# Kernel optimization log

Measured on AMD Instinct MI355X. Metric: run time of the kernel, lower is better.

## Reference

```python
import jax, jax.numpy as jnp
import numpy as np

B, S, HID = 2, 2048, 4096
NH, NKV, D = 32, 8, 128
GROUPS = NH // NKV  # 4 query heads per KV head
THETA = 10000.0
MAX_SEQ = 4096


def _rope_tables():
    half = D // 2
    inv_freq = 1.0 / (THETA ** (np.arange(half, dtype=np.float32) / half))
    t = np.arange(MAX_SEQ, dtype=np.float32)
    freqs = np.outer(t, inv_freq)  # [MAX_SEQ, D//2]
    return jnp.asarray(np.cos(freqs)), jnp.asarray(np.sin(freqs))

ROPE_COS, ROPE_SIN = _rope_tables()


def _apply_rope(x, cos, sin):
    # x: [B, S, H, D]; cos/sin: [S, D//2]; half-split (NeoX) rotation as in _apply_rope_inline
    half = x.shape[-1] // 2
    x0, x1 = x[..., :half], x[..., half:]
    c = cos[None, :, None, :]
    s = sin[None, :, None, :]
    return jnp.concatenate([x0 * c - x1 * s, x0 * s + x1 * c], axis=-1)


def setup_inputs() -> dict:
    key = jax.random.key(0)
    ks = jax.random.split(key, 5)
    wscale = 1.0 / np.sqrt(HID).astype(np.float32)  # keep activations O(1)
    return {
        "x": jax.random.normal(ks[0], (B, S, HID), dtype=jnp.float32),
        "positions": jnp.arange(S, dtype=jnp.int32),
        "w_q": jax.random.normal(ks[1], (NH * D, HID), dtype=jnp.float32) * wscale,
        "w_k": jax.random.normal(ks[2], (NKV * D, HID), dtype=jnp.float32) * wscale,
        "w_v": jax.random.normal(ks[3], (NKV * D, HID), dtype=jnp.float32) * wscale,
        "w_o": jax.random.normal(ks[4], (HID, NH * D), dtype=jnp.float32) * wscale,
    }


def reference(x, positions, w_q, w_k, w_v, w_o):
    cos = ROPE_COS[positions]  # [S, D//2]
    sin = ROPE_SIN[positions]
    # Separate Q/K/V projections (no bias), as in the training forward()
    q = (x @ w_q.T).reshape(B, S, NH, D)
    k = (x @ w_k.T).reshape(B, S, NKV, D)
    v = (x @ w_v.T).reshape(B, S, NKV, D)
    q = _apply_rope(q, cos, sin)
    k = _apply_rope(k, cos, sin)
    # [B, H, S, D] layout
    q = q.transpose(0, 2, 1, 3)
    k = k.transpose(0, 2, 1, 3)
    v = v.transpose(0, 2, 1, 3)
    # GQA: group query heads over shared KV heads instead of repeating K/V
    qg = q.reshape(B, NKV, GROUPS, S, D)
    scale = 1.0 / jnp.sqrt(jnp.float32(D))
    scores = jnp.einsum("bkgqd,bkmd->bkgqm", qg, k) * scale  # [B, NKV, G, Sq, Skv]
    causal = jnp.tril(jnp.ones((S, S), dtype=bool))
    scores = jnp.where(causal[None, None, None], scores, jnp.float32(-jnp.inf))
    probs = jax.nn.softmax(scores, axis=-1)
    ctx = jnp.einsum("bkgqm,bkmd->bkgqd", probs, v)  # [B, NKV, G, S, D]
    ctx = ctx.reshape(B, NH, S, D).transpose(0, 2, 1, 3).reshape(B, S, NH * D)
    return ctx @ w_o.T
```

## Files before the change

### kernel.cpp

```cpp
#include <hip/hip_runtime.h>
#include <math.h>

typedef short s16x8 __attribute__((ext_vector_type(8)));
typedef float f32x4 __attribute__((ext_vector_type(4)));
typedef unsigned u32x4 __attribute__((ext_vector_type(4)));
typedef unsigned short u16;

#define S_LEN 2048
#define HID_DIM 4096
#define NH_Q 32
#define NKV_H 8
#define DHEAD 128

__device__ __forceinline__ u16 f2bf(float f) {
  unsigned u = __builtin_bit_cast(unsigned, f);
  u += 0x7fffu + ((u >> 16) & 1u);
  return (u16)(u >> 16);
}

__device__ __forceinline__ void gload16(const u16* g, u16* l) {
  __builtin_amdgcn_global_load_lds(
      (const __attribute__((address_space(1))) void*)g,
      (__attribute__((address_space(3))) void*)l, 16, 0, 0);
}

__global__ void cvt_kernel(const float* __restrict__ in, u16* __restrict__ out, int n4) {
  int stride = gridDim.x * blockDim.x;
  for (int i = blockIdx.x * blockDim.x + threadIdx.x; i < n4; i += stride) {
    float4 f = ((const float4*)in)[i];
    uint2 o;
    o.x = (unsigned)f2bf(f.x) | ((unsigned)f2bf(f.y) << 16);
    o.y = (unsigned)f2bf(f.z) | ((unsigned)f2bf(f.w) << 16);
    ((uint2*)out)[i] = o;
  }
}

__global__ void cvt_all_kernel(const float* __restrict__ x, const float* __restrict__ wq,
                               const float* __restrict__ wk, const float* __restrict__ wv,
                               const float* __restrict__ wo, u16* __restrict__ x_bf,
                               u16* __restrict__ wqkv_bf, u16* __restrict__ wo_bf,
                               const int* __restrict__ positions, float* __restrict__ cos_t,
                               float* __restrict__ sin_t, int with_wo) {
  const int R0 = 4194304, R1 = 8388608, R2 = 9437184, R3 = 10485760, R4 = 14680064;
  const int cvt_end = with_wo ? R4 : R3;
  const int rope_units = 32768;
  const int total = cvt_end + rope_units;
  const int stride = gridDim.x * blockDim.x;
  for (int i = blockIdx.x * blockDim.x + threadIdx.x; i < total; i += stride) {
    if (i < cvt_end) {
      const float* src;
      u16* dst;
      int off;
      if (i < R0)      { src = x;  dst = x_bf;               off = i; }
      else if (i < R1) { src = wq; dst = wqkv_bf;            off = i - R0; }
      else if (i < R2) { src = wk; dst = wqkv_bf + 16777216; off = i - R1; }
      else if (i < R3) { src = wv; dst = wqkv_bf + 20971520; off = i - R2; }
      else             { src = wo; dst = wo_bf;              off = i - R3; }
      float4 f = ((const float4*)src)[off];
      uint2 o;
      o.x = (unsigned)f2bf(f.x) | ((unsigned)f2bf(f.y) << 16);
      o.y = (unsigned)f2bf(f.z) | ((unsigned)f2bf(f.w) << 16);
      ((uint2*)dst)[off] = o;
    } else {
      int base = (i - cvt_end) * 4;
#pragma unroll
      for (int e = 0; e < 4; ++e) {
        int idx = base + e;
        int s = idx >> 6, j = idx & 63;
        float pos = (float)positions[s];
        float inv = expf(-(float)j * (9.210340371976184f / 64.0f));
        float sv, cv;
        sincosf(pos * inv, &sv, &cv);
        cos_t[idx] = cv;
        sin_t[idx] = sv;
      }
    }
  }
}

__global__ void rope_table_kernel(const int* __restrict__ positions,
                                  float* __restrict__ cos_t, float* __restrict__ sin_t) {
  int idx = blockIdx.x * 256 + threadIdx.x;
  if (idx >= S_LEN * 64) return;
  int s = idx >> 6, j = idx & 63;
  float pos = (float)positions[s];
  float inv = expf(-(float)j * (9.210340371976184f / 64.0f));
  float sv, cv;
  sincosf(pos * inv, &sv, &cv);
  cos_t[idx] = cv;
  sin_t[idx] = sv;
}

template<int EPI>
__global__ __launch_bounds__(512, 2) void gemmp_kernel(
    const u16* __restrict__ A, const u16* __restrict__ B,
    void* __restrict__ outp, int M, int N, int K,
    const float* __restrict__ cos_t, const float* __restrict__ sin_t) {
  __shared__ u16 LDS[73728];
  const int t = threadIdx.x;
  const int wave = t >> 6, lane = t & 63;
  const int l15 = lane & 15, lhi = lane >> 4;
  const int wr = wave >> 2, wc = wave & 3;
  const int gx = gridDim.x;
  const int nwg = gx * gridDim.y;
  const int id = blockIdx.y * gx + blockIdx.x;
  const int xcd = id & 7, cid = id >> 3;
  const int npx = gx >> 3;
  const int gy = nwg / gx;
  const int bxi = xcd * npx + cid / gy;
  const int byi = cid % gy;
  const int bm = byi * 128, bn = bxi * 256;

  const int sw = l15 & 7;
  int aoff[4][2], boff[2][2];
#pragma unroll
  for (int q = 0; q < 4; ++q)
#pragma unroll
    for (int ks = 0; ks < 2; ++ks)
      aoff[q][ks] = wr * 4096 + (q * 16 + l15) * 64 + (((ks << 2) + lhi) ^ sw) * 8;
#pragma unroll
  for (int f = 0; f < 2; ++f)
#pragma unroll
    for (int ks = 0; ks < 2; ++ks)
      boff[f][ks] = (f * 64 + wc * 16 + l15) * 64 + (((ks << 2) + lhi) ^ sw) * 8;

  const int lr1 = t >> 3;
  const int cs1 = ((t & 7) ^ (lr1 & 7)) * 8;
  const int ldsw = wave * 512;

  const f32x4 fz = {0.f, 0.f, 0.f, 0.f};
  f32x4 acc[4][4];
#pragma unroll
  for (int mf = 0; mf < 4; ++mf)
#pragma unroll
    for (int nf = 0; nf < 4; ++nf) acc[mf][nf] = fz;

  auto stageA = [&](int tile, int buf) {
    const size_t kb = (size_t)tile * 64;
    gload16(A + (size_t)(bm + lr1) * K + kb + cs1, &LDS[buf * 8192 + ldsw]);
    gload16(A + (size_t)(bm + 64 + lr1) * K + kb + cs1, &LDS[buf * 8192 + 4096 + ldsw]);
  };
  auto stageB = [&](int tile, int h, int buf) {
    const size_t kb = (size_t)tile * 64;
    gload16(B + (size_t)(bn + h * 128 + lr1) * K + kb + cs1,
            &LDS[24576 + buf * 16384 + h * 8192 + ldsw]);
    gload16(B + (size_t)(bn + h * 128 + 64 + lr1) * K + kb + cs1,
            &LDS[24576 + buf * 16384 + h * 8192 + 4096 + ldsw]);
  };

  s16x8 afr0[4][2], afr1[4][2];
  s16x8 bfr00[2][2], bfr01[2][2];
  s16x8 bfr10[2][2], bfr11[2][2];

#define READ_TILE(SET, BUF)                                                \
  do {                                                                     \
    const int _b = (BUF);                                                  \
    const int _ba = _b * 8192;                                             \
    _Pragma("unroll") for (int q = 0; q < 4; ++q)                          \
      _Pragma("unroll") for (int ks = 0; ks < 2; ++ks)                     \
        afr##SET[q][ks] = *(const s16x8*)&LDS[_ba + aoff[q][ks]];          \
    const int _b0 = 24576 + _b * 16384;                                    \
    _Pragma("unroll") for (int f = 0; f < 2; ++f)                          \
      _Pragma("unroll") for (int ks = 0; ks < 2; ++ks)                     \
        bfr0##SET[f][ks] = *(const s16x8*)&LDS[_b0 + boff[f][ks]];         \
    const int _b1 = _b0 + 8192;                                            \
    _Pragma("unroll") for (int f = 0; f < 2; ++f)                          \
      _Pragma("unroll") for (int ks = 0; ks < 2; ++ks)                     \
        bfr1##SET[f][ks] = *(const s16x8*)&LDS[_b1 + boff[f][ks]];         \
  } while (0)

#define MFMA_HALF(SET, NFH, BH)                                            \
  do {                                                                     \
    __builtin_amdgcn_s_setprio(1);                                         \
    _Pragma("unroll") for (int q = 0; q < 4; ++q)                          \
      _Pragma("unroll") for (int f = 0; f < 2; ++f)                        \
        _Pragma("unroll") for (int ks = 0; ks < 2; ++ks)                   \
          acc[q][(NFH)*2 + f] = __builtin_amdgcn_mfma_f32_16x16x32_bf16(   \
              afr##SET[q][ks], bfr##BH##SET[f][ks], acc[q][(NFH)*2 + f],   \
              0, 0, 0);                                                    \
    __builtin_amdgcn_s_setprio(0);                                         \
  } while (0)

#define TILE_BODY(SET, OSET, TT)                                           \
  do {                                                                     \
    const int _tt = (TT);                                                  \
    const bool _s2 = _tt + 2 < nt;                                         \
    if (_s2) { stageA(_tt + 2, nx2); stageB(_tt + 2, 0, nx2); }            \
    asm volatile("s_waitcnt lgkmcnt(0)" ::: "memory");                     \
    __builtin_amdgcn_sched_barrier(0);                                     \
    MFMA_HALF(SET, 0, 0);                                                  \
    if (_s2) stageB(_tt + 2, 1, nx2);                                      \
    if (_tt + 1 < nt) {                                                    \
      if (_s2) { asm volatile("s_waitcnt vmcnt(6)" ::: "memory"); }        \
      else     { asm volatile("s_waitcnt vmcnt(0)" ::: "memory"); }        \
      __builtin_amdgcn_sched_barrier(0);                                   \
      __builtin_amdgcn_s_barrier();                                        \
      __builtin_amdgcn_sched_barrier(0);                                   \
      READ_TILE(OSET, nxt1);                                               \
    }                                                                      \
    MFMA_HALF(SET, 1, 1);                                                  \
    nxt1 = nx2;                                                            \
    nx2 = (nx2 == 2) ? 0 : nx2 + 1;                                        \
  } while (0)

  const int nt = K >> 6;
  stageA(0, 0); stageB(0, 0, 0); stageB(0, 1, 0);
  stageA(1, 1); stageB(1, 0, 1); stageB(1, 1, 1);
  asm volatile("s_waitcnt vmcnt(6)" ::: "memory");
  __builtin_amdgcn_sched_barrier(0);
  __builtin_amdgcn_s_barrier();
  __builtin_amdgcn_sched_barrier(0);
  READ_TILE(0, 0);

  int nxt1 = 1, nx2 = 2;
  for (int tt = 0; tt < nt; tt += 2) {
    TILE_BODY(0, 1, tt);
    TILE_BODY(1, 0, tt + 1);
  }
#undef TILE_BODY
#undef MFMA_HALF
#undef READ_TILE

  u16* qp = (u16*)outp;
  u16* kp = qp + 16777216;
  u16* vp = kp + 4194304;
  if (bn < 5120) {
    const bool isQ = bn < 4096;
    u16* O = isQ ? qp : kp;
    const int hb = isQ ? (bn >> 7) : ((bn - 4096) >> 7);
    const int Hh = isQ ? NH_Q : NKV_H;
    const int j = wc * 16 + l15;
#pragma unroll
    for (int mf = 0; mf < 4; ++mf) {
      int rb = bm + wr * 64 + mf * 16 + lhi * 4;
#pragma unroll
      for (int p = 0; p < 2; ++p) {
        int head = hb + p;
#pragma unroll
        for (int i = 0; i < 4; ++i) {
          int m = rb + i;
          int b = m >> 11, srw = m & 2047;
          float c = cos_t[srw * 64 + j];
          float s = sin_t[srw * 64 + j];
          float x0 = acc[mf][2 * p][i];
          float x1 = acc[mf][2 * p + 1][i];
          size_t base = ((size_t)(b * Hh + head) * S_LEN + srw) * DHEAD;
          O[base + j] = f2bf(x0 * c - x1 * s);
          O[base + j + 64] = f2bf(x0 * s + x1 * c);
        }
      }
    }
  } else {
#pragma unroll
    for (int mf = 0; mf < 4; ++mf) {
      int rb = bm + wr * 64 + mf * 16 + lhi * 4;
#pragma unroll
      for (int nfi = 0; nfi < 4; ++nfi) {
        int colrel = bn - 5120 + wc * 16 + (nfi & 1) * 64 + (nfi >> 1) * 128 + l15;
        int head = colrel >> 7, d = colrel & 127;
#pragma unroll
        for (int i = 0; i < 4; ++i) {
          int m = rb + i;
          int b = m >> 11, srw = m & 2047;
          vp[((size_t)(b * NKV_H + head) * DHEAD + d) * S_LEN + srw] = f2bf(acc[mf][nfi][i]);
        }
      }
    }
  }
}

__global__ __launch_bounds__(512, 1) void gemmo_kernel(
    const u16* __restrict__ A, const u16* __restrict__ B,
    float* __restrict__ C, int M, int N, int K) {
  __shared__ u16 LDS[49152];
  const int t = threadIdx.x;
  const int wave = t >> 6, lane = t & 63;
  const int l15 = lane & 15, lhi = lane >> 4;
  const int wr = wave >> 1, wc = wave & 1;
  const int gx = gridDim.x;
  const int nwg = gx * gridDim.y;
  const int id = blockIdx.y * gx + blockIdx.x;
  const int xcd = id & 7, cid = id >> 3;
  const int npx = gx >> 3;
  const int gy = nwg / gx;
  const int bxi = xcd * npx + cid / gy;
  const int byi = cid % gy;
  const int bm = byi * 256, bn = bxi * 256;

  const int sw = (l15 >> 1) & 3;
  int aoff[4], boff[8];
#pragma unroll
  for (int mf = 0; mf < 4; ++mf)
    aoff[mf] = (wr * 64 + mf * 16 + l15) * 32 + ((lhi ^ sw) << 3);
#pragma unroll
  for (int nf = 0; nf < 8; ++nf)
    boff[nf] = (wc * 128 + nf * 16 + l15) * 32 + ((lhi ^ sw) << 3);

  const int r0 = t >> 2;
  const int cs = (((t & 3) ^ ((t >> 3) & 3)) << 3);

  const f32x4 fz = {0.f, 0.f, 0.f, 0.f};
  f32x4 acc[4][8];
#pragma unroll
  for (int mf = 0; mf < 4; ++mf)
#pragma unroll
    for (int nf = 0; nf < 8; ++nf) acc[mf][nf] = fz;

  auto stageA = [&](int tile, int buf) {
    const size_t kb = (size_t)tile * 32;
    const u16* s0 = A + (size_t)(bm + r0) * K + kb + cs;
    u16* d = &LDS[buf * 8192 + (wave << 9)];
    gload16(s0, d);
    gload16(s0 + (size_t)128 * K, d + 4096);
  };
  auto stageB = [&](int tile, int buf) {
    const size_t kb = (size_t)tile * 32;
    const u16* s0 = B + (size_t)(bn + r0) * K + kb + cs;
    u16* d = &LDS[24576 + buf * 8192 + (wave << 9)];
    gload16(s0, d);
    gload16(s0 + (size_t)128 * K, d + 4096);
  };

  s16x8 afr0[4], afr1[4], bfr0[8], bfr1[8];

#define READ_TILE(SET, BUF)                                                \
  do {                                                                     \
    const int _ab = (BUF) * 8192;                                          \
    const int _bb = 24576 + (BUF) * 8192;                                  \
    _Pragma("unroll") for (int mf = 0; mf < 4; ++mf)                       \
      afr##SET[mf] = *(const s16x8*)&LDS[_ab + aoff[mf]];                  \
    _Pragma("unroll") for (int nf = 0; nf < 8; ++nf)                       \
      bfr##SET[nf] = *(const s16x8*)&LDS[_bb + boff[nf]];                  \
  } while (0)

#define MFMA_HALF(SET, H)                                                  \
  do {                                                                     \
    __builtin_amdgcn_s_setprio(1);                                         \
    _Pragma("unroll") for (int mf = 0; mf < 4; ++mf)                       \
      _Pragma("unroll") for (int nf = 0; nf < 4; ++nf)                     \
        acc[mf][(H)*4 + nf] = __builtin_amdgcn_mfma_f32_16x16x32_bf16(     \
            afr##SET[mf], bfr##SET[(H)*4 + nf], acc[mf][(H)*4 + nf],       \
            0, 0, 0);                                                      \
    __builtin_amdgcn_s_setprio(0);                                         \
  } while (0)

#define TILE_BODY(SET, OSET, TT)                                           \
  do {                                                                     \
    const int _tt = (TT);                                                  \
    const bool _s2 = _tt + 2 < nt;                                         \
    if (_s2) stageA(_tt + 2, nx2);                                         \
    asm volatile("s_waitcnt lgkmcnt(0)" ::: "memory");                     \
    __builtin_amdgcn_sched_barrier(0);                                     \
    MFMA_HALF(SET, 0);                                                     \
    if (_s2) stageB(_tt + 2, nx2);                                         \
    if (_tt + 1 < nt) {                                                    \
      if (_s2) { asm volatile("s_waitcnt vmcnt(4)" ::: "memory"); }        \
      else     { asm volatile("s_waitcnt vmcnt(0)" ::: "memory"); }        \
      __builtin_amdgcn_sched_barrier(0);                                   \
      __builtin_amdgcn_s_barrier();                                        \
      __builtin_amdgcn_sched_barrier(0);                                   \
      READ_TILE(OSET, nxt1);                                               \
    }                                                                      \
    MFMA_HALF(SET, 1);                                                     \
    nxt1 = nx2;                                                            \
    nx2 = (nx2 == 2) ? 0 : nx2 + 1;                                        \
  } while (0)

  const int nt = K >> 5;
  stageA(0, 0); stageB(0, 0);
  stageA(1, 1); stageB(1, 1);
  asm volatile("s_waitcnt vmcnt(4)" ::: "memory");
  __builtin_amdgcn_sched_barrier(0);
  __builtin_amdgcn_s_barrier();
  __builtin_amdgcn_sched_barrier(0);
  READ_TILE(0, 0);

  int nxt1 = 1, nx2 = 2;
  for (int tt = 0; tt < nt; tt += 2) {
    TILE_BODY(0, 1, tt);
    TILE_BODY(1, 0, tt + 1);
  }
#undef TILE_BODY
#undef MFMA_HALF
#undef READ_TILE

#pragma unroll
  for (int mf = 0; mf < 4; ++mf) {
    int rb = bm + wr * 64 + mf * 16 + lhi * 4;
#pragma unroll
    for (int nf = 0; nf < 8; ++nf) {
      int col = bn + wc * 128 + nf * 16 + l15;
#pragma unroll
      for (int i = 0; i < 4; ++i) C[(size_t)(rb + i) * N + col] = acc[mf][nf][i];
    }
  }
}

template<int EPI, bool ABF16, bool BBF16>
__global__ __launch_bounds__(256) void gemm_kernel(
    const void* __restrict__ Aptr, const void* __restrict__ Bptr,
    void* __restrict__ outp, void* __restrict__ outp2, int M, int N, int K,
    const float* __restrict__ cos_t, const float* __restrict__ sin_t, int Hh) {
  __shared__ u16 As[128][72];
  __shared__ u16 Bs[128][72];
  const int t = threadIdx.x;
  const int wave = t >> 6, lane = t & 63;
  const int l15 = lane & 15, lhi = lane >> 4;
  const int gx = gridDim.x;
  const int nwg = gx * gridDim.y;
  const int id = blockIdx.y * gx + blockIdx.x;
  const int swz = (id & 7) * (nwg >> 3) + (id >> 3);
  const int bm = (swz / gx) * 128, bn = (swz % gx) * 128;

  const f32x4 fz = {0.f, 0.f, 0.f, 0.f};
  f32x4 acc[2][8];
#pragma unroll
  for (int a0 = 0; a0 < 2; ++a0)
#pragma unroll
    for (int b0 = 0; b0 < 8; ++b0) acc[a0][b0] = fz;

  for (int kt = 0; kt < K; kt += 64) {
    __syncthreads();
    if (ABF16) {
      const u16* A = (const u16*)Aptr;
#pragma unroll
      for (int p = 0; p < 4; ++p) {
        int row = p * 32 + (t >> 3), kc = (t & 7) * 8;
        *(s16x8*)&As[row][kc] = *(const s16x8*)(A + (size_t)(bm + row) * K + kt + kc);
      }
    } else {
      const float* A = (const float*)Aptr;
#pragma unroll
      for (int p = 0; p < 8; ++p) {
        int row = p * 16 + (t >> 4), kc = (t & 15) * 4;
        float4 f = *(const float4*)(A + (size_t)(bm + row) * K + kt + kc);
        unsigned* dst = (unsigned*)&As[row][kc];
        dst[0] = (unsigned)f2bf(f.x) | ((unsigned)f2bf(f.y) << 16);
        dst[1] = (unsigned)f2bf(f.z) | ((unsigned)f2bf(f.w) << 16);
      }
    }
    if (BBF16) {
      const u16* Bw = (const u16*)Bptr;
#pragma unroll
      for (int p = 0; p < 4; ++p) {
        int row = p * 32 + (t >> 3), kc = (t & 7) * 8;
        *(s16x8*)&Bs[row][kc] = *(const s16x8*)(Bw + (size_t)(bn + row) * K + kt + kc);
      }
    } else {
      const float* Bw = (const float*)Bptr;
#pragma unroll
      for (int p = 0; p < 8; ++p) {
        int row = p * 16 + (t >> 4), kc = (t & 15) * 4;
        float4 f = *(const float4*)(Bw + (size_t)(bn + row) * K + kt + kc);
        unsigned* dst = (unsigned*)&Bs[row][kc];
        dst[0] = (unsigned)f2bf(f.x) | ((unsigned)f2bf(f.y) << 16);
        dst[1] = (unsigned)f2bf(f.z) | ((unsigned)f2bf(f.w) << 16);
      }
    }
    __syncthreads();
#pragma unroll
    for (int ks = 0; ks < 2; ++ks) {
      s16x8 bfr[8];
#pragma unroll
      for (int nf = 0; nf < 8; ++nf)
        bfr[nf] = *(const s16x8*)&Bs[nf * 16 + l15][ks * 32 + lhi * 8];
#pragma unroll
      for (int mf = 0; mf < 2; ++mf) {
        s16x8 a = *(const s16x8*)&As[wave * 32 + mf * 16 + l15][ks * 32 + lhi * 8];
#pragma unroll
        for (int nf = 0; nf < 8; ++nf)
          acc[mf][nf] = __builtin_amdgcn_mfma_f32_16x16x32_bf16(a, bfr[nf], acc[mf][nf], 0, 0, 0);
      }
    }
  }

  if (EPI == 0) {
    float* C = (float*)outp;
#pragma unroll
    for (int mf = 0; mf < 2; ++mf)
#pragma unroll
      for (int nf = 0; nf < 8; ++nf) {
        int col = bn + nf * 16 + l15;
        int rb = bm + wave * 32 + mf * 16 + lhi * 4;
#pragma unroll
        for (int i = 0; i < 4; ++i) C[(size_t)(rb + i) * N + col] = acc[mf][nf][i];
      }
  } else if (EPI == 2) {
    u16* O = (u16*)outp;
    int h = bn >> 7;
#pragma unroll
    for (int mf = 0; mf < 2; ++mf)
#pragma unroll
      for (int nf = 0; nf < 4; ++nf) {
        int j = nf * 16 + l15;
        int rb = bm + wave * 32 + mf * 16 + lhi * 4;
#pragma unroll
        for (int i = 0; i < 4; ++i) {
          int m = rb + i;
          int b = m >> 11, srow = m & 2047;
          float c = cos_t[srow * 64 + j];
          float s = sin_t[srow * 64 + j];
          float x0 = acc[mf][nf][i];
          float x1 = acc[mf][nf + 4][i];
          size_t base = ((size_t)(b * Hh + h) * S_LEN + srow) * DHEAD;
          O[base + j] = f2bf(x0 * c - x1 * s);
          O[base + j + 64] = f2bf(x0 * s + x1 * c);
        }
      }
  } else {
    u16* O = (u16*)outp;
#pragma unroll
    for (int mf = 0; mf < 2; ++mf)
#pragma unroll
      for (int nf = 0; nf < 8; ++nf) {
        int col = bn + nf * 16 + l15;
        int h = col >> 7, d = col & 127;
        int rb = bm + wave * 32 + mf * 16 + lhi * 4;
#pragma unroll
        for (int i = 0; i < 4; ++i) {
          int m = rb + i;
          int b = m >> 11, srow = m & 2047;
          O[((size_t)(b * Hh + h) * DHEAD + d) * S_LEN + srow] = f2bf(acc[mf][nf][i]);
        }
      }
  }
}

#define KIDX(r, c) (((r) * 128 + (c)) ^ (((r) & 7) << 3))
#define VIDX(d, kv) (((d) * 64 + (kv)) ^ (((d) & 7) << 3))
__global__ __launch_bounds__(512) void attn_kernel(
    const u16* __restrict__ q, const u16* __restrict__ k, const u16* __restrict__ vt,
    u16* __restrict__ ctx) {
  __shared__ u16 Ks[64 * 128];
  __shared__ u16 Vts[128 * 64];

  const int t = threadIdx.x;
  const int wave = t >> 6, lane = t & 63;
  const int l15 = lane & 15, lhi = lane >> 4;
  const int pi = blockIdx.x, h = blockIdx.y, b = blockIdx.z;
  const int kvh = h >> 2;
  const int qsub[2] = {pi, 15 - pi};
  const int ntiles = 32 - 2 * pi;

  const u16* qb = q + ((size_t)(b * NH_Q + h)) * S_LEN * DHEAD;
  const u16* kb = k + ((size_t)(b * NKV_H + kvh)) * S_LEN * DHEAD;
  const u16* vtb = vt + ((size_t)(b * NKV_H + kvh)) * DHEAD * S_LEN;

  s16x8 qf[2][4];
#pragma unroll
  for (int s = 0; s < 2; ++s)
#pragma unroll
    for (int ks = 0; ks < 4; ++ks)
      qf[s][ks] = *(const s16x8*)(qb + (size_t)(qsub[s] * 128 + wave * 16 + l15) * DHEAD +
                                  ks * 32 + lhi * 8);

  const f32x4 fz = {0.f, 0.f, 0.f, 0.f};
  f32x4 acc[2][8];
#pragma unroll
  for (int s = 0; s < 2; ++s)
#pragma unroll
    for (int i = 0; i < 8; ++i) acc[s][i] = fz;
  float mrow[2] = {-INFINITY, -INFINITY};
  float lsum[2] = {0.f, 0.f};

  const float scale = 0.08838834764831845f;

  const int sl0 = l15 | (((2 * lhi) & 3) << 4);
  const int sl1 = sl0 | 16;
  const bool hisel = (lhi & 2) != 0;

  const int krow = t >> 3, kd0 = (t & 7) * 16;
  const int vrow = t >> 2, vk0 = (t & 3) * 16;
  s16x8 kr0, kr1, vr0, vr1;
  {
    const u16* p = kb + (size_t)krow * DHEAD + kd0;
    kr0 = *(const s16x8*)p;
    kr1 = *(const s16x8*)(p + 8);
    const u16* pv = vtb + (size_t)vrow * S_LEN + vk0;
    vr0 = *(const s16x8*)pv;
    vr1 = *(const s16x8*)(pv + 8);
  }

  for (int tt = 0; tt < ntiles; ++tt) {
    __syncthreads();
    *(s16x8*)&Ks[KIDX(krow, kd0)] = kr0;
    *(s16x8*)&Ks[KIDX(krow, kd0 + 8)] = kr1;
    *(s16x8*)&Vts[VIDX(vrow, vk0)] = vr0;
    *(s16x8*)&Vts[VIDX(vrow, vk0 + 8)] = vr1;
    __syncthreads();
    if (tt + 1 < ntiles) {
      const u16* p = kb + (size_t)((tt + 1) * 64 + krow) * DHEAD + kd0;
      kr0 = *(const s16x8*)p;
      kr1 = *(const s16x8*)(p + 8);
      const u16* pv = vtb + (size_t)vrow * S_LEN + (tt + 1) * 64 + vk0;
      vr0 = *(const s16x8*)pv;
      vr1 = *(const s16x8*)(pv + 8);
    }

    const int kc_base = tt * 64;
#pragma unroll
    for (int s = 0; s < 2; ++s) {
      const int wmin = qsub[s] * 128 + wave * 16;
      if (kc_base > wmin + 15) continue;
      f32x4 sacc[4];
#pragma unroll
      for (int i = 0; i < 4; ++i) sacc[i] = fz;
      __builtin_amdgcn_s_setprio(1);
#pragma unroll
      for (int ks = 0; ks < 4; ++ks) {
#pragma unroll
        for (int nf = 0; nf < 4; ++nf) {
          s16x8 kf = *(const s16x8*)&Ks[KIDX(nf * 16 + l15, ks * 32 + lhi * 8)];
          sacc[nf] = __builtin_amdgcn_mfma_f32_16x16x32_bf16(kf, qf[s][ks], sacc[nf], 0, 0, 0);
        }
      }
      __builtin_amdgcn_s_setprio(0);

      const int qg = wmin + l15;
      float pmax = -INFINITY;
      if (kc_base + 63 > wmin) {
#pragma unroll
        for (int nf = 0; nf < 4; ++nf)
#pragma unroll
          for (int i = 0; i < 4; ++i) {
            int kv = kc_base + nf * 16 + lhi * 4 + i;
            float sv = sacc[nf][i] * scale;
            sv = (kv <= qg) ? sv : -INFINITY;
            sacc[nf][i] = sv;
            pmax = fmaxf(pmax, sv);
          }
      } else {
#pragma unroll
        for (int nf = 0; nf < 4; ++nf)
#pragma unroll
          for (int i = 0; i < 4; ++i) {
            float sv = sacc[nf][i] * scale;
            sacc[nf][i] = sv;
            pmax = fmaxf(pmax, sv);
          }
      }
      pmax = fmaxf(pmax, __shfl_xor(pmax, 16, 64));
      pmax = fmaxf(pmax, __shfl_xor(pmax, 32, 64));

      if (!__all(pmax <= mrow[s] + 8.0f)) {
        float mnew = fmaxf(mrow[s], pmax);
        float alpha = __expf(mrow[s] - mnew);
        mrow[s] = mnew;
        lsum[s] *= alpha;
#pragma unroll
        for (int i = 0; i < 4; ++i) {
          float al = __shfl(alpha, (lane & 48) | (lhi * 4 + i), 64);
#pragma unroll
          for (int df = 0; df < 8; ++df) acc[s][df][i] *= al;
        }
      }

      float rsum = 0.f;
      unsigned pk[4][2];
#pragma unroll
      for (int nf = 0; nf < 4; ++nf) {
        float p0 = __expf(sacc[nf][0] - mrow[s]);
        float p1 = __expf(sacc[nf][1] - mrow[s]);
        float p2 = __expf(sacc[nf][2] - mrow[s]);
        float p3 = __expf(sacc[nf][3] - mrow[s]);
        rsum += (p0 + p1) + (p2 + p3);
        pk[nf][0] = (unsigned)f2bf(p0) | ((unsigned)f2bf(p1) << 16);
        pk[nf][1] = (unsigned)f2bf(p2) | ((unsigned)f2bf(p3) << 16);
      }
      rsum += __shfl_xor(rsum, 16, 64);
      rsum += __shfl_xor(rsum, 32, 64);
      lsum[s] += rsum;

      s16x8 pa[2];
#pragma unroll
      for (int ph = 0; ph < 2; ++ph) {
        unsigned lo0 = __shfl((int)pk[2 * ph][0], sl0, 64);
        unsigned hi0 = __shfl((int)pk[2 * ph + 1][0], sl0, 64);
        unsigned lo1 = __shfl((int)pk[2 * ph][1], sl0, 64);
        unsigned hi1 = __shfl((int)pk[2 * ph + 1][1], sl0, 64);
        unsigned lo2 = __shfl((int)pk[2 * ph][0], sl1, 64);
        unsigned hi2 = __shfl((int)pk[2 * ph + 1][0], sl1, 64);
        unsigned lo3 = __shfl((int)pk[2 * ph][1], sl1, 64);
        unsigned hi3 = __shfl((int)pk[2 * ph + 1][1], sl1, 64);
        u32x4 w;
        w[0] = hisel ? hi0 : lo0;
        w[1] = hisel ? hi1 : lo1;
        w[2] = hisel ? hi2 : lo2;
        w[3] = hisel ? hi3 : lo3;
        pa[ph] = __builtin_bit_cast(s16x8, w);
      }

      __builtin_amdgcn_s_setprio(1);
#pragma unroll
      for (int ph = 0; ph < 2; ++ph) {
#pragma unroll
        for (int df = 0; df < 8; ++df) {
          s16x8 bb = *(const s16x8*)&Vts[VIDX(df * 16 + l15, ph * 32 + lhi * 8)];
          acc[s][df] = __builtin_amdgcn_mfma_f32_16x16x32_bf16(pa[ph], bb, acc[s][df], 0, 0, 0);
        }
      }
      __builtin_amdgcn_s_setprio(0);
    }
  }

#pragma unroll
  for (int s = 0; s < 2; ++s) {
    float rl = 1.0f / lsum[s];
#pragma unroll
    for (int i = 0; i < 4; ++i) {
      float rli = __shfl(rl, (lane & 48) | (lhi * 4 + i), 64);
      int m = b * S_LEN + qsub[s] * 128 + wave * 16 + lhi * 4 + i;
#pragma unroll
      for (int df = 0; df < 8; ++df) {
        int col = h * DHEAD + df * 16 + l15;
        ctx[(size_t)m * (NH_Q * DHEAD) + col] = f2bf(acc[s][df][i] * rli);
      }
    }
  }
}

extern "C" void kernel_launch(void* const* d_in, const int* in_sizes, int n_in,
                              void* d_out, int out_size, void* d_ws, size_t ws_size,
                              hipStream_t stream) {
  const float* x = (const float*)d_in[0];
  const int* positions = (const int*)d_in[1];
  const float* wq = (const float*)d_in[2];
  const float* wk = (const float*)d_in[3];
  const float* wv = (const float*)d_in[4];
  const float* wo = (const float*)d_in[5];
  float* out = (float*)d_out;

  char* ws = (char*)d_ws;
  const size_t MB1 = 1048576;
  const size_t SZ_X = 33554432;
  const size_t SZ_WQKV = 50331648;
  const size_t SZ_WO = 33554432;
  const size_t SZ_Q = 33554432;
  const size_t SZ_WK = 8388608;
  const size_t NEED_FULL = MB1 + SZ_X + SZ_WQKV + SZ_Q + 2 * SZ_WK;
  const size_t NEED_WO = NEED_FULL + SZ_WO;

  float* cos_t = (float*)ws;
  float* sin_t = (float*)(ws + MB1 / 2);

  if (ws_size >= NEED_WO) {
    char* p = ws + MB1;
    u16* x_bf = (u16*)p;    p += SZ_X;
    u16* wqkv_bf = (u16*)p; p += SZ_WQKV;
    u16* wo_bf = (u16*)p;   p += SZ_WO;
    u16* q_ws = (u16*)p;    p += SZ_Q;
    u16* k_ws = (u16*)p;    p += SZ_WK;
    u16* v_ws = (u16*)p;    p += SZ_WK;
    u16* ctx_ws = x_bf;

    cvt_all_kernel<<<2048, 256, 0, stream>>>(x, wq, wk, wv, wo, x_bf, wqkv_bf, wo_bf,
                                             positions, cos_t, sin_t, 1);
    gemmp_kernel<5><<<dim3(24, 32), 512, 0, stream>>>(
        x_bf, wqkv_bf, q_ws, 4096, 6144, 4096, cos_t, sin_t);
    attn_kernel<<<dim3(8, 32, 2), 512, 0, stream>>>(q_ws, k_ws, v_ws, ctx_ws);
    gemmo_kernel<<<dim3(16, 16), 512, 0, stream>>>(
        ctx_ws, wo_bf, out, 4096, 4096, 4096);
  } else if (ws_size >= NEED_FULL) {
    char* p = ws + MB1;
    u16* x_bf = (u16*)p;    p += SZ_X;
    u16* wqkv_bf = (u16*)p; p += SZ_WQKV;
    u16* q_ws = (u16*)p;    p += SZ_Q;
    u16* k_ws = (u16*)p;    p += SZ_WK;
    u16* v_ws = (u16*)p;    p += SZ_WK;
    u16* ctx_ws = x_bf;

    cvt_all_kernel<<<2048, 256, 0, stream>>>(x, wq, wk, wv, nullptr, x_bf, wqkv_bf, nullptr,
                                             positions, cos_t, sin_t, 0);
    gemmp_kernel<5><<<dim3(24, 32), 512, 0, stream>>>(
        x_bf, wqkv_bf, q_ws, 4096, 6144, 4096, cos_t, sin_t);
    cvt_kernel<<<2048, 256, 0, stream>>>(wo, wqkv_bf, 4194304);
    attn_kernel<<<dim3(8, 32, 2), 512, 0, stream>>>(q_ws, k_ws, v_ws, ctx_ws);
    gemmo_kernel<<<dim3(16, 16), 512, 0, stream>>>(
        ctx_ws, wqkv_bf, out, 4096, 4096, 4096);
  } else {
    u16* q_ws = (u16*)(ws + MB1);
    u16* k_ws = (u16*)(ws + MB1 + SZ_Q);
    u16* v_ws = (u16*)(ws + MB1 + SZ_Q + SZ_WK);
    u16* ctx_ws = (u16*)(ws + MB1 + SZ_Q + 2 * SZ_WK);

    rope_table_kernel<<<512, 256, 0, stream>>>(positions, cos_t, sin_t);
    gemm_kernel<2, false, false><<<dim3(32, 32), 256, 0, stream>>>(
        x, wq, q_ws, nullptr, 4096, 4096, 4096, cos_t, sin_t, NH_Q);
    gemm_kernel<2, false, false><<<dim3(8, 32), 256, 0, stream>>>(
        x, wk, k_ws, nullptr, 4096, 1024, 4096, cos_t, sin_t, NKV_H);
    gemm_kernel<4, false, false><<<dim3(8, 32), 256, 0, stream>>>(
        x, wv, v_ws, nullptr, 4096, 1024, 4096, nullptr, nullptr, NKV_H);
    attn_kernel<<<dim3(8, 32, 2), 512, 0, stream>>>(q_ws, k_ws, v_ws, ctx_ws);
    gemm_kernel<0, true, false><<<dim3(32, 32), 256, 0, stream>>>(
        ctx_ws, wo, out, nullptr, 4096, 4096, 4096, nullptr, nullptr, 0);
  }
}
```

Measured before the change: 518.6 us.

## Restructure output-projection GEMM pipeline to 4-buffer two-tile steps

The output projection GEMM moves from a 3-stage ring buffer with interleaved half-MFMA/LDS-read scheduling to a 4-buffer LDS scheme that processes two K-tiles per iteration with one barrier. Both tiles' fragments are read up front and staging of the next two tiles is issued early. The aim is to halve barrier count and give the loads more time in flight. In exchange it uses more LDS, holds more register fragments, and the full vmcnt(0) wait at the end of each step may expose global load latency.

```diff
diff --git a/kernel.cpp b/kernel.cpp
--- a/kernel.cpp
+++ b/kernel.cpp
@@ -272,7 +272,7 @@
 __global__ __launch_bounds__(512, 1) void gemmo_kernel(
     const u16* __restrict__ A, const u16* __restrict__ B,
     float* __restrict__ C, int M, int N, int K) {
-  __shared__ u16 LDS[49152];
+  __shared__ u16 LDS[65536];
   const int t = threadIdx.x;
   const int wave = t >> 6, lane = t & 63;
   const int l15 = lane & 15, lhi = lane >> 4;
@@ -306,83 +306,67 @@
 #pragma unroll
     for (int nf = 0; nf < 8; ++nf) acc[mf][nf] = fz;
 
-  auto stageA = [&](int tile, int buf) {
+  auto stageT = [&](int tile) {
+    const int buf = tile & 3;
     const size_t kb = (size_t)tile * 32;
-    const u16* s0 = A + (size_t)(bm + r0) * K + kb + cs;
-    u16* d = &LDS[buf * 8192 + (wave << 9)];
-    gload16(s0, d);
-    gload16(s0 + (size_t)128 * K, d + 4096);
+    const u16* sa = A + (size_t)(bm + r0) * K + kb + cs;
+    u16* da = &LDS[buf * 8192 + (wave << 9)];
+    gload16(sa, da);
+    gload16(sa + (size_t)128 * K, da + 4096);
+    const u16* sb = B + (size_t)(bn + r0) * K + kb + cs;
+    u16* db = &LDS[32768 + buf * 8192 + (wave << 9)];
+    gload16(sb, db);
+    gload16(sb + (size_t)128 * K, db + 4096);
   };
-  auto stageB = [&](int tile, int buf) {
-    const size_t kb = (size_t)tile * 32;
-    const u16* s0 = B + (size_t)(bn + r0) * K + kb + cs;
-    u16* d = &LDS[24576 + buf * 8192 + (wave << 9)];
-    gload16(s0, d);
-    gload16(s0 + (size_t)128 * K, d + 4096);
-  };
 
   s16x8 afr0[4], afr1[4], bfr0[8], bfr1[8];
 
-#define READ_TILE(SET, BUF)                                                \
+#define READ_T(SET, BUF)                                                   \
   do {                                                                     \
     const int _ab = (BUF) * 8192;                                          \
-    const int _bb = 24576 + (BUF) * 8192;                                  \
+    const int _bb = 32768 + (BUF) * 8192;                                  \
     _Pragma("unroll") for (int mf = 0; mf < 4; ++mf)                       \
       afr##SET[mf] = *(const s16x8*)&LDS[_ab + aoff[mf]];                  \
     _Pragma("unroll") for (int nf = 0; nf < 8; ++nf)                       \
       bfr##SET[nf] = *(const s16x8*)&LDS[_bb + boff[nf]];                  \
   } while (0)
 
-#define MFMA_HALF(SET, H)                                                  \
+#define MFMA_T(SET)                                                        \
   do {                                                                     \
     __builtin_amdgcn_s_setprio(1);                                         \
     _Pragma("unroll") for (int mf = 0; mf < 4; ++mf)                       \
-      _Pragma("unroll") for (int nf = 0; nf < 4; ++nf)                     \
-        acc[mf][(H)*4 + nf] = __builtin_amdgcn_mfma_f32_16x16x32_bf16(     \
-            afr##SET[mf], bfr##SET[(H)*4 + nf], acc[mf][(H)*4 + nf],       \
-            0, 0, 0);                                                      \
+      _Pragma("unroll") for (int nf = 0; nf < 8; ++nf)                     \
+        acc[mf][nf] = __builtin_amdgcn_mfma_f32_16x16x32_bf16(             \
+            afr##SET[mf], bfr##SET[nf], acc[mf][nf], 0, 0, 0);             \
     __builtin_amdgcn_s_setprio(0);                                         \
   } while (0)
 
-#define TILE_BODY(SET, OSET, TT)                                           \
-  do {                                                                     \
-    const int _tt = (TT);                                                  \
-    const bool _s2 = _tt + 2 < nt;                                         \
-    if (_s2) stageA(_tt + 2, nx2);                                         \
-    asm volatile("s_waitcnt lgkmcnt(0)" ::: "memory");                     \
-    __builtin_amdgcn_sched_barrier(0);                                     \
-    MFMA_HALF(SET, 0);                                                     \
-    if (_s2) stageB(_tt + 2, nx2);                                         \
-    if (_tt + 1 < nt) {                                                    \
-      if (_s2) { asm volatile("s_waitcnt vmcnt(4)" ::: "memory"); }        \
-      else     { asm volatile("s_waitcnt vmcnt(0)" ::: "memory"); }        \
-      __builtin_amdgcn_sched_barrier(0);                                   \
-      __builtin_amdgcn_s_barrier();                                        \
-      __builtin_amdgcn_sched_barrier(0);                                   \
-      READ_TILE(OSET, nxt1);                                               \
-    }                                                                      \
-    MFMA_HALF(SET, 1);                                                     \
-    nxt1 = nx2;                                                            \
-    nx2 = (nx2 == 2) ? 0 : nx2 + 1;                                        \
-  } while (0)
-
   const int nt = K >> 5;
-  stageA(0, 0); stageB(0, 0);
-  stageA(1, 1); stageB(1, 1);
-  asm volatile("s_waitcnt vmcnt(4)" ::: "memory");
+  stageT(0); stageT(1);
+  asm volatile("s_waitcnt vmcnt(0)" ::: "memory");
   __builtin_amdgcn_sched_barrier(0);
   __builtin_amdgcn_s_barrier();
   __builtin_amdgcn_sched_barrier(0);
-  READ_TILE(0, 0);
-
-  int nxt1 = 1, nx2 = 2;
-  for (int tt = 0; tt < nt; tt += 2) {
-    TILE_BODY(0, 1, tt);
-    TILE_BODY(1, 0, tt + 1);
-  }
-#undef TILE_BODY
-#undef MFMA_HALF
-#undef READ_TILE
+
+  for (int u = 0; u < nt; u += 2) {
+    const bool s2 = u + 2 < nt, s3 = u + 3 < nt;
+    if (s2) stageT(u + 2);
+    READ_T(0, u & 3);
+    if (s3) stageT(u + 3);
+    READ_T(1, (u + 1) & 3);
+    asm volatile("s_waitcnt lgkmcnt(12)" ::: "memory");
+    __builtin_amdgcn_sched_barrier(0);
+    MFMA_T(0);
+    asm volatile("s_waitcnt lgkmcnt(0)" ::: "memory");
+    __builtin_amdgcn_sched_barrier(0);
+    MFMA_T(1);
+    asm volatile("s_waitcnt vmcnt(0)" ::: "memory");
+    __builtin_amdgcn_sched_barrier(0);
+    __builtin_amdgcn_s_barrier();
+    __builtin_amdgcn_sched_barrier(0);
+  }
+#undef READ_T
+#undef MFMA_T
 
 #pragma unroll
   for (int mf = 0; mf < 4; ++mf) {
```

Measured after the change: 524.0 us. No clear change (+1.0%).
